# Kernel tuning notes

Hardware: AMD Instinct MI355X
Metric: run time of the kernel (lower is better)

Reference implementation:

```python
import jax, jax.numpy as jnp
import numpy as np

B, M, NV, H, D = 32, 64, 65, 960, 480
ROUNDS = 5
SCALE = D ** -0.5


def _self_att(x, m, qw, qb):
    # x: [B, P, Q, C] attention over Q within each (b, p); m: [B, P, Q]
    qkv = x @ qw.T + qb                      # [B,P,Q,3C]
    q, k, v = jnp.split(qkv, 3, axis=-1)
    # torch builds mask@mask^T/C from a C-times repeated mask == outer product of mask values
    am = m[..., :, None] * m[..., None, :]   # [B,P,Q,Q]
    a = jnp.einsum('bpqc,bpkc->bpqk', q, k) * SCALE
    a = jnp.where(am == 0, -10000.0, a)
    a = jax.nn.softmax(a, axis=-1)
    return jnp.einsum('bpqk,bpkc->bpqc', a, v)


def _attn_logits(x, mask, qw, qb):
    # Attention_logits.forward: attend over value axis, then over key axis
    x = _self_att(x, mask, qw, qb)
    x = _self_att(jnp.swapaxes(x, 1, 2), jnp.swapaxes(mask, 1, 2), qw, qb)
    return jnp.swapaxes(x, 1, 2)


def _biaffine(x1, x2, W, lw, lb):
    # torch.nn.Bilinear (no bias) on the MxN outer grid + Linear(cat(x1,x2)) with bias,
    # computed without materializing the repeated [B,M,N,2D] tensor.
    d = x1.shape[-1]
    bil = jnp.einsum('bmi,oij,bnj->bmno', x1, W, x2)
    lin = (x1 @ lw[:, :d].T)[:, :, None, :] + (x2 @ lw[:, d:].T)[:, None, :, :] + lb
    return bil + lin


def _rounds(key, value, km, vm, W, lw, lb, fw, fb, qw, qb):
    # shared structure of type_classifier / single_classifier (rounds=5, max pooling)
    lm = km[:, :, None] * vm[:, None, :]     # [B,M,N]
    logits = None
    for i in range(ROUNDS):
        logits = _biaffine(key, value, W, lw, lb)          # [B,M,N,out]
        if i < ROUNDS - 1:
            logits = logits @ fw.T + fb                    # [B,M,N,D]
            logits = _attn_logits(logits, lm, qw, qb)
            key = key + logits.max(axis=2)                 # max-pool over values
            value = value + logits.max(axis=1)             # max-pool over keys
        else:
            logits = logits * lm[..., None]
    return logits


def setup_inputs() -> dict:
    root = jax.random.key(0)
    ks = list(jax.random.split(root, 40))
    it = iter(ks)
    nrm = lambda sh, s=0.02: (jax.random.normal(next(it), sh, jnp.float32) * s)
    key = jax.random.normal(next(it), (B, M, H), jnp.float32)
    value = jax.random.normal(next(it), (B, NV, H), jnp.float32)
    klen = jax.random.randint(next(it), (B,), 1, M + 1)
    key_mask = (jnp.arange(M)[None, :] < klen[:, None]).astype(jnp.float32)
    vlen = jax.random.randint(next(it), (B,), 1, NV + 1)
    value_mask = (jnp.arange(NV)[None, :] < vlen[:, None]).astype(jnp.float32)
    return dict(
        key=key, value=value, key_mask=key_mask, value_mask=value_mask,
        w_kt=nrm((D, H)), b_kt=nrm((D,)), w_vt=nrm((D, H)), b_vt=nrm((D,)),
        w_km=nrm((D, H)), b_km=nrm((D,)), w_vm=nrm((D, H)), b_vm=nrm((D,)),
        w_ks=nrm((D, H)), b_ks=nrm((D,)), w_vs=nrm((D, H)), b_vs=nrm((D,)),
        bt_W=nrm((3, D, D)), bt_lw=nrm((3, 2 * D)), bt_lb=nrm((3,)),
        bi_W=nrm((2, D, D)), bi_lw=nrm((2, 2 * D)), bi_lb=nrm((2,)),
        w_ffnt=nrm((D, 3)), b_ffnt=nrm((D,)), w_ffn=nrm((D, 2)), b_ffn=nrm((D,)),
        qkvt_w=nrm((3 * D, D)), qkvt_b=nrm((3 * D,)),
        qkv_w=nrm((3 * D, D)), qkv_b=nrm((3 * D,)),
        w_cls=nrm((2, 2 * D)), b_cls=nrm((2,)),
    )


def reference(key, value, key_mask, value_mask,
              w_kt, b_kt, w_vt, b_vt, w_km, b_km, w_vm, b_vm,
              w_ks, b_ks, w_vs, b_vs,
              bt_W, bt_lw, bt_lb, bi_W, bi_lw, bi_lb,
              w_ffnt, b_ffnt, w_ffn, b_ffn,
              qkvt_w, qkvt_b, qkv_w, qkv_b, w_cls, b_cls):
    # --- type classifier ---
    kt = key @ w_kt.T + b_kt
    vt = value @ w_vt.T + b_vt
    type_logits = _rounds(kt, vt, key_mask, value_mask,
                          bt_W, bt_lw, bt_lb, w_ffnt, b_ffnt, qkvt_w, qkvt_b)  # [B,M,NV,3]
    # drop type token from values
    v1 = value[:, 1:, :]
    vm1 = value_mask[:, 1:]
    type_token = jax.nn.softmax(type_logits[:, :, 0], axis=-1)   # [B,M,3]
    key_type = jnp.argmax(type_token, axis=-1)
    type_single = key_type == 1
    # --- multi classifier (masks unused, as in original) ---
    km_f = key @ w_km.T + b_km
    vm_f = v1 @ w_vm.T + b_vm
    multi_logits = ((km_f @ w_cls[:, :D].T)[:, :, None, :]
                    + (vm_f @ w_cls[:, D:].T)[:, None, :, :] + b_cls)  # [B,M,M? -> B,64,64,2]
    # --- single classifier with key mask restricted to single-link keys ---
    km2 = (key_mask.astype(bool) & type_single).astype(key_mask.dtype)
    ks_f = key @ w_ks.T + b_ks
    vs_f = v1 @ w_vs.T + b_vs
    single_logits = _rounds(ks_f, vs_f, km2, vm1,
                            bi_W, bi_lw, bi_lb, w_ffn, b_ffn, qkv_w, qkv_b)  # [B,64,64,2]
    return (type_logits, multi_logits, single_logits)
```

## Files before the change

### kernel.cpp

```cpp
#include <hip/hip_runtime.h>
#include <math.h>

constexpr int NB = 32;
constexpr int NM = 64;
constexpr int NNV = 65;
constexpr int NH = 960;
constexpr int ND = 480;
constexpr float ATT_SCALE = 0.045643546458763842f;

constexpr int OF_Pq = 0;
constexpr int OF_cq = 4320;
constexpr int OF_Q2 = 5760;
constexpr int OF_V2 = OF_Q2 + 2*1440;
constexpr int OF_dq = 10080;
constexpr int OF_dv = OF_dq + 2*480;
constexpr int OF_S  = 11520;
constexpr int OF_u  = 11529;
constexpr int OF_r  = 11532;
constexpr int OF_w  = 11535;
constexpr int FOLD_SZ = 11552;

typedef float f32x4 __attribute__((ext_vector_type(4)));
typedef short s16x8 __attribute__((ext_vector_type(8)));

__device__ __forceinline__ float wave_sum(float v) {
#pragma unroll
  for (int d = 32; d; d >>= 1) v += __shfl_xor(v, d);
  return v;
}

__device__ __forceinline__ void split_bf16(float x, short& hi, short& lo) {
  union { float f; unsigned u; } a; a.f = x;
  unsigned uh = a.u + 0x7fffu + ((a.u >> 16) & 1u);
  hi = (short)(uh >> 16);
  union { unsigned u; float f; } b; b.u = ((unsigned)(unsigned short)hi) << 16;
  union { float f; unsigned u; } c; c.f = x - b.f;
  unsigned ul = c.u + 0x7fffu + ((c.u >> 16) & 1u);
  lo = (short)(ul >> 16);
}

struct ProjCfg {
  const float* X; const float* W; const float* bias; float* C;
  int R; int x0; int rpb; int xbs;
};
struct Proj6 { ProjCfg c[6]; };

constexpr int KP = 40;

__global__ __launch_bounds__(256) void k_projM(Proj6 P, int K)
{
  __shared__ unsigned short As_hi[64][KP], As_lo[64][KP];
  __shared__ unsigned short Bs_hi[48][KP], Bs_lo[48][KP];
  int p = blockIdx.x, total = gridDim.x;
  int q = total >> 3, r = total & 7;
  int xk = p & 7, idx = p >> 3;
  int lgc = (xk < r) ? (xk * (q + 1) + idx) : (r * (q + 1) + (xk - r) * q + idx);
  int mp = lgc / 10, nx = lgc - mp * 10;
  ProjCfg cfg; int my;
  if      (mp < 32)  { cfg = P.c[0]; my = mp; }
  else if (mp < 65)  { cfg = P.c[1]; my = mp - 32; }
  else if (mp < 97)  { cfg = P.c[2]; my = mp - 65; }
  else if (mp < 129) { cfg = P.c[3]; my = mp - 97; }
  else if (mp < 161) { cfg = P.c[4]; my = mp - 129; }
  else               { cfg = P.c[5]; my = mp - 161; }
  const int m0 = my * 64, n0 = nx * 48;
  const int tid = threadIdx.x;
  const int l6 = tid & 63, w = tid >> 6;
  const int lr = tid >> 2, kc = (tid & 3) * 8;
  const float* Arow = nullptr;
  {
    int rr = m0 + lr;
    if (rr < cfg.R) {
      int b = rr / cfg.rpb, r2 = rr - b * cfg.rpb;
      Arow = cfg.X + (size_t)b * cfg.xbs + (size_t)(cfg.x0 + r2) * K;
    }
  }
  const float* Brow = (lr < 48) ? (cfg.W + (size_t)(n0 + lr) * K) : nullptr;
  const int fr = l6 & 15, fk = (l6 >> 4) * 8;
  f32x4 acc0 = {0.f, 0.f, 0.f, 0.f}, acc1 = acc0, acc2 = acc0;
  for (int k0 = 0; k0 < K; k0 += 32) {
    float xs[8] = {0.f, 0.f, 0.f, 0.f, 0.f, 0.f, 0.f, 0.f};
    if (Arow) {
      float4 a0 = *(const float4*)(Arow + k0 + kc);
      float4 a1 = *(const float4*)(Arow + k0 + kc + 4);
      xs[0] = a0.x; xs[1] = a0.y; xs[2] = a0.z; xs[3] = a0.w;
      xs[4] = a1.x; xs[5] = a1.y; xs[6] = a1.z; xs[7] = a1.w;
    }
    s16x8 vh, vl;
#pragma unroll
    for (int e = 0; e < 8; ++e) { short h, lo2; split_bf16(xs[e], h, lo2); vh[e] = h; vl[e] = lo2; }
    *(s16x8*)&As_hi[lr][kc] = vh;
    *(s16x8*)&As_lo[lr][kc] = vl;
    if (Brow) {
      float4 b0 = *(const float4*)(Brow + k0 + kc);
      float4 b1 = *(const float4*)(Brow + k0 + kc + 4);
      float ys[8] = {b0.x, b0.y, b0.z, b0.w, b1.x, b1.y, b1.z, b1.w};
      s16x8 wh, wl;
#pragma unroll
      for (int e = 0; e < 8; ++e) { short h, lo2; split_bf16(ys[e], h, lo2); wh[e] = h; wl[e] = lo2; }
      *(s16x8*)&Bs_hi[lr][kc] = wh;
      *(s16x8*)&Bs_lo[lr][kc] = wl;
    }
    __syncthreads();
    s16x8 ah = *(const s16x8*)&As_hi[16 * w + fr][fk];
    s16x8 al = *(const s16x8*)&As_lo[16 * w + fr][fk];
    {
      s16x8 bh = *(const s16x8*)&Bs_hi[fr][fk];
      s16x8 bl = *(const s16x8*)&Bs_lo[fr][fk];
      acc0 = __builtin_amdgcn_mfma_f32_16x16x32_bf16(ah, bh, acc0, 0, 0, 0);
      acc0 = __builtin_amdgcn_mfma_f32_16x16x32_bf16(ah, bl, acc0, 0, 0, 0);
      acc0 = __builtin_amdgcn_mfma_f32_16x16x32_bf16(al, bh, acc0, 0, 0, 0);
    }
    {
      s16x8 bh = *(const s16x8*)&Bs_hi[16 + fr][fk];
      s16x8 bl = *(const s16x8*)&Bs_lo[16 + fr][fk];
      acc1 = __builtin_amdgcn_mfma_f32_16x16x32_bf16(ah, bh, acc1, 0, 0, 0);
      acc1 = __builtin_amdgcn_mfma_f32_16x16x32_bf16(ah, bl, acc1, 0, 0, 0);
      acc1 = __builtin_amdgcn_mfma_f32_16x16x32_bf16(al, bh, acc1, 0, 0, 0);
    }
    {
      s16x8 bh = *(const s16x8*)&Bs_hi[32 + fr][fk];
      s16x8 bl = *(const s16x8*)&Bs_lo[32 + fr][fk];
      acc2 = __builtin_amdgcn_mfma_f32_16x16x32_bf16(ah, bh, acc2, 0, 0, 0);
      acc2 = __builtin_amdgcn_mfma_f32_16x16x32_bf16(ah, bl, acc2, 0, 0, 0);
      acc2 = __builtin_amdgcn_mfma_f32_16x16x32_bf16(al, bh, acc2, 0, 0, 0);
    }
    __syncthreads();
  }
#pragma unroll
  for (int c = 0; c < 3; ++c) {
    f32x4 av = (c == 0) ? acc0 : (c == 1) ? acc1 : acc2;
    int n = n0 + 16 * c + fr;
    float bv = cfg.bias[n];
#pragma unroll
    for (int g = 0; g < 4; ++g) {
      int rr = m0 + 16 * w + (l6 >> 4) * 4 + g;
      if (rr < cfg.R) cfg.C[(size_t)rr * ND + n] = av[g] + bv;
    }
  }
}

__global__ __launch_bounds__(256) void k_tmpM(
    const float* __restrict__ Key, const float* __restrict__ W,
    float* __restrict__ T, int O)
{
  __shared__ unsigned short As_hi[64][KP], As_lo[64][KP];
  __shared__ unsigned short Bs_hi[48][KP], Bs_lo[48][KP];
  const int n0 = blockIdx.x * 48;
  const int o = blockIdx.y, b = blockIdx.z;
  const int tid = threadIdx.x;
  const int l6 = tid & 63, w = tid >> 6;
  const int lr = tid >> 2, kc = (tid & 3) * 8;
  const float* Arow = Key + (size_t)b * NM * ND + (size_t)lr * ND;
  const float* Wo = W + (size_t)o * ND * ND;
  const int fr = l6 & 15, fk = (l6 >> 4) * 8;
  f32x4 acc0 = {0.f, 0.f, 0.f, 0.f}, acc1 = acc0, acc2 = acc0;
  for (int k0 = 0; k0 < ND; k0 += 32) {
    {
      float4 a0 = *(const float4*)(Arow + k0 + kc);
      float4 a1 = *(const float4*)(Arow + k0 + kc + 4);
      float xs[8] = {a0.x, a0.y, a0.z, a0.w, a1.x, a1.y, a1.z, a1.w};
      s16x8 vh, vl;
#pragma unroll
      for (int e = 0; e < 8; ++e) { short h, lo2; split_bf16(xs[e], h, lo2); vh[e] = h; vl[e] = lo2; }
      *(s16x8*)&As_hi[lr][kc] = vh;
      *(s16x8*)&As_lo[lr][kc] = vl;
    }
    if (lr < 48) {
      s16x8 wh, wl;
#pragma unroll
      for (int e = 0; e < 8; ++e) {
        float x = Wo[(size_t)(k0 + kc + e) * ND + n0 + lr];
        short h, lo2; split_bf16(x, h, lo2); wh[e] = h; wl[e] = lo2;
      }
      *(s16x8*)&Bs_hi[lr][kc] = wh;
      *(s16x8*)&Bs_lo[lr][kc] = wl;
    }
    __syncthreads();
    s16x8 ah = *(const s16x8*)&As_hi[16 * w + fr][fk];
    s16x8 al = *(const s16x8*)&As_lo[16 * w + fr][fk];
    {
      s16x8 bh = *(const s16x8*)&Bs_hi[fr][fk];
      s16x8 bl = *(const s16x8*)&Bs_lo[fr][fk];
      acc0 = __builtin_amdgcn_mfma_f32_16x16x32_bf16(ah, bh, acc0, 0, 0, 0);
      acc0 = __builtin_amdgcn_mfma_f32_16x16x32_bf16(ah, bl, acc0, 0, 0, 0);
      acc0 = __builtin_amdgcn_mfma_f32_16x16x32_bf16(al, bh, acc0, 0, 0, 0);
    }
    {
      s16x8 bh = *(const s16x8*)&Bs_hi[16 + fr][fk];
      s16x8 bl = *(const s16x8*)&Bs_lo[16 + fr][fk];
      acc1 = __builtin_amdgcn_mfma_f32_16x16x32_bf16(ah, bh, acc1, 0, 0, 0);
      acc1 = __builtin_amdgcn_mfma_f32_16x16x32_bf16(ah, bl, acc1, 0, 0, 0);
      acc1 = __builtin_amdgcn_mfma_f32_16x16x32_bf16(al, bh, acc1, 0, 0, 0);
    }
    {
      s16x8 bh = *(const s16x8*)&Bs_hi[32 + fr][fk];
      s16x8 bl = *(const s16x8*)&Bs_lo[32 + fr][fk];
      acc2 = __builtin_amdgcn_mfma_f32_16x16x32_bf16(ah, bh, acc2, 0, 0, 0);
      acc2 = __builtin_amdgcn_mfma_f32_16x16x32_bf16(ah, bl, acc2, 0, 0, 0);
      acc2 = __builtin_amdgcn_mfma_f32_16x16x32_bf16(al, bh, acc2, 0, 0, 0);
    }
    __syncthreads();
  }
  float* C = T + ((size_t)(b * O + o) * NM) * ND;
#pragma unroll
  for (int c = 0; c < 3; ++c) {
    f32x4 av = (c == 0) ? acc0 : (c == 1) ? acc1 : acc2;
    int n = n0 + 16 * c + fr;
#pragma unroll
    for (int g = 0; g < 4; ++g) {
      int rr = 16 * w + (l6 >> 4) * 4 + g;
      C[(size_t)rr * ND + n] = av[g];
    }
  }
}

template <int O, int NVX>
__global__ __launch_bounds__(256) void k_bilatt0(
    const float* __restrict__ T, const float* __restrict__ Val,
    const float* __restrict__ linK, const float* __restrict__ linV,
    const float* __restrict__ lb, const float* __restrict__ F,
    const float* __restrict__ km, const float* __restrict__ vm,
    int vmOff, int vmStride, float* __restrict__ Y1)
{
  __shared__ float Ls[NVX][3];
  __shared__ float STs[NVX][3];
  __shared__ float hs[NVX], gs[NVX], mkj[NVX];
  __shared__ float Pm[NVX][66];
  __shared__ float rmx[NVX][3];
  __shared__ float rsum[NVX][3];
  __shared__ float ry[NVX][3][3];
  __shared__ float lvs[NVX][3];
  const int b = blockIdx.x >> 6, m = blockIdx.x & 63;
  const int tid = threadIdx.x;
  const int lane = tid & 63, w = tid >> 6;

  for (int j = tid; j < NVX; j += 256) {
    mkj[j] = vm[b * vmStride + vmOff + j];
#pragma unroll
    for (int o = 0; o < O; ++o) lvs[j][o] = linV[((size_t)b * NVX + j) * O + o];
  }
  float4 tsr[O][2];
#pragma unroll
  for (int o = 0; o < O; ++o) {
    const float4* trow = (const float4*)(T + (((size_t)b * O + o) * NM + m) * (size_t)ND);
    tsr[o][0] = trow[lane];
    tsr[o][1] = (lane < 56) ? trow[64 + lane] : make_float4(0.f, 0.f, 0.f, 0.f);
  }
  float lk[O];
#pragma unroll
  for (int o = 0; o < O; ++o) lk[o] = linK[((size_t)b * NM + m) * O + o] + lb[o];
  const float gm = km[b * NM + m];
  const bool gz = (gm == 0.f);

  for (int n = w; n < NVX; n += 4) {
    const float4* vrow = (const float4*)(Val + ((size_t)b * NVX + n) * (size_t)ND);
    float4 v0 = vrow[lane];
    float4 v1 = (lane < 56) ? vrow[64 + lane] : make_float4(0.f, 0.f, 0.f, 0.f);
    float a[3] = {0.f, 0.f, 0.f};
#pragma unroll
    for (int o = 0; o < O; ++o) {
      a[o] = v0.x * tsr[o][0].x + v0.y * tsr[o][0].y + v0.z * tsr[o][0].z + v0.w * tsr[o][0].w
           + v1.x * tsr[o][1].x + v1.y * tsr[o][1].y + v1.z * tsr[o][1].z + v1.w * tsr[o][1].w;
    }
#pragma unroll
    for (int o = 0; o < O; ++o) a[o] = wave_sum(a[o]);
    if (lane == 0) {
#pragma unroll
      for (int o = 0; o < O; ++o) Ls[n][o] = a[o] + lk[o] + lvs[n][o];
      if (O == 2) Ls[n][2] = 0.f;
    }
  }
  __syncthreads();
  const float* Sm = F + OF_S;
  const float u0 = F[OF_u], u1 = F[OF_u + 1], u2 = F[OF_u + 2];
  const float r0 = F[OF_r], r1 = F[OF_r + 1], r2 = F[OF_r + 2];
  const float wc = F[OF_w];
  if (tid < NVX) {
    int j = tid;
    float t0 = Ls[j][0], t1 = Ls[j][1], t2 = Ls[j][2];
    STs[j][0] = t0 * Sm[0] + t1 * Sm[3] + t2 * Sm[6];
    STs[j][1] = t0 * Sm[1] + t1 * Sm[4] + t2 * Sm[7];
    STs[j][2] = t0 * Sm[2] + t1 * Sm[5] + t2 * Sm[8];
    hs[j] = t0 * u0 + t1 * u1 + t2 * u2;
    gs[j] = t0 * r0 + t1 * r1 + t2 * r2;
  }
  __syncthreads();
  const bool act = tid < NVX * 3;
  int i = 0, qq = 0, jlo = 0, jhi = 0;
  float st0 = 0, st1 = 0, st2 = 0, hi = 0;
  bool rowz = true;
  if (act) {
    i = tid / 3; qq = tid - i * 3;
    jlo = qq * 22; jhi = (jlo + 22 < NVX) ? jlo + 22 : NVX;
    st0 = STs[i][0]; st1 = STs[i][1]; st2 = STs[i][2]; hi = hs[i];
    rowz = gz || (mkj[i] == 0.f);
    float mx = -3.0e38f;
    for (int j = jlo; j < jhi; ++j) {
      float s = st0 * Ls[j][0] + st1 * Ls[j][1] + hi + gs[j] + wc;
      if (O == 3) s += st2 * Ls[j][2];
      s = (rowz || mkj[j] == 0.f) ? -10000.f : ATT_SCALE * s;
      Pm[i][j] = s;
      mx = fmaxf(mx, s);
    }
    rmx[i][qq] = mx;
  }
  __syncthreads();
  if (act) {
    float mx = fmaxf(fmaxf(rmx[i][0], rmx[i][1]), rmx[i][2]);
    float sum = 0.f, y0 = 0.f, y1 = 0.f, y2 = 0.f;
    for (int j = jlo; j < jhi; ++j) {
      float pp = __expf(Pm[i][j] - mx);
      sum += pp; y0 += pp * Ls[j][0]; y1 += pp * Ls[j][1];
      if (O == 3) y2 += pp * Ls[j][2];
    }
    rsum[i][qq] = sum; ry[i][qq][0] = y0; ry[i][qq][1] = y1; ry[i][qq][2] = y2;
  }
  __syncthreads();
  if (tid < NVX) {
    int ii = tid;
    float sum = rsum[ii][0] + rsum[ii][1] + rsum[ii][2];
    float y0 = ry[ii][0][0] + ry[ii][1][0] + ry[ii][2][0];
    float y1 = ry[ii][0][1] + ry[ii][1][1] + ry[ii][2][1];
    float y2 = ry[ii][0][2] + ry[ii][1][2] + ry[ii][2][2];
    float inv = 1.f / sum;
    size_t ob = (((size_t)b * NM + m) * NVX + ii) * O;
    Y1[ob + 0] = y0 * inv;
    Y1[ob + 1] = y1 * inv;
    if (O == 3) Y1[ob + 2] = y2 * inv;
  }
}

template <int O, int NVX>
__global__ __launch_bounds__(256) void k_att1vupd(
    const float* __restrict__ Y1, float* __restrict__ Y2,
    const float* __restrict__ F,
    const float* __restrict__ km, const float* __restrict__ vm,
    int vmOff, int vmStride,
    float* __restrict__ valb, const float* __restrict__ lw,
    float* __restrict__ linV)
{
  __shared__ float Ys1[NM][3];
  __shared__ float STs[NM][3];
  __shared__ float hs[NM], gs[NM], mkm[NM];
  __shared__ float Pm[NM][66];
  __shared__ float rmx[NM][3];
  __shared__ float rsum[NM][3];
  __shared__ float ry[NM][3][3];
  __shared__ float Ys2[NM][3];
  __shared__ float vrow[ND];
  const int b = blockIdx.x / NVX, n = blockIdx.x - b * NVX;
  const int tid = threadIdx.x;
  for (int u = tid; u < NM * O; u += 256) {
    int mm = u % NM, o = u / NM;
    Ys1[mm][o] = Y1[(((size_t)b * NM + mm) * NVX + n) * O + o];
  }
  if (tid < NM) {
    mkm[tid] = km[b * NM + tid];
    if (O == 2) Ys1[tid][2] = 0.f;
  }
  const float gm = vm[b * vmStride + vmOff + n];
  const bool gz = (gm == 0.f);
  __syncthreads();
  const float* Sm = F + OF_S + 16;
  const float u0 = F[OF_u + 16], u1 = F[OF_u + 17], u2 = F[OF_u + 18];
  const float r0 = F[OF_r + 16], r1 = F[OF_r + 17], r2 = F[OF_r + 18];
  const float wc = F[OF_w + 16];
  if (tid < NM) {
    int j = tid;
    float t0 = Ys1[j][0], t1 = Ys1[j][1], t2 = Ys1[j][2];
    STs[j][0] = t0 * Sm[0] + t1 * Sm[3] + t2 * Sm[6];
    STs[j][1] = t0 * Sm[1] + t1 * Sm[4] + t2 * Sm[7];
    STs[j][2] = t0 * Sm[2] + t1 * Sm[5] + t2 * Sm[8];
    hs[j] = t0 * u0 + t1 * u1 + t2 * u2;
    gs[j] = t0 * r0 + t1 * r1 + t2 * r2;
  }
  __syncthreads();
  const bool act = tid < NM * 3;
  int i = 0, qq = 0, jlo = 0, jhi = 0;
  float st0 = 0, st1 = 0, st2 = 0, hi = 0;
  bool rowz = true;
  if (act) {
    i = tid / 3; qq = tid - i * 3;
    jlo = qq * 22; jhi = (jlo + 22 < NM) ? jlo + 22 : NM;
    st0 = STs[i][0]; st1 = STs[i][1]; st2 = STs[i][2]; hi = hs[i];
    rowz = gz || (mkm[i] == 0.f);
    float mx = -3.0e38f;
    for (int j = jlo; j < jhi; ++j) {
      float s = st0 * Ys1[j][0] + st1 * Ys1[j][1] + hi + gs[j] + wc;
      if (O == 3) s += st2 * Ys1[j][2];
      s = (rowz || mkm[j] == 0.f) ? -10000.f : ATT_SCALE * s;
      Pm[i][j] = s;
      mx = fmaxf(mx, s);
    }
    rmx[i][qq] = mx;
  }
  __syncthreads();
  if (act) {
    float mx = fmaxf(fmaxf(rmx[i][0], rmx[i][1]), rmx[i][2]);
    float sum = 0.f, y0 = 0.f, y1 = 0.f, y2 = 0.f;
    for (int j = jlo; j < jhi; ++j) {
      float pp = __expf(Pm[i][j] - mx);
      sum += pp; y0 += pp * Ys1[j][0]; y1 += pp * Ys1[j][1];
      if (O == 3) y2 += pp * Ys1[j][2];
    }
    rsum[i][qq] = sum; ry[i][qq][0] = y0; ry[i][qq][1] = y1; ry[i][qq][2] = y2;
  }
  __syncthreads();
  if (tid < NM) {
    int ii = tid;
    float sum = rsum[ii][0] + rsum[ii][1] + rsum[ii][2];
    float y0 = ry[ii][0][0] + ry[ii][1][0] + ry[ii][2][0];
    float y1 = ry[ii][0][1] + ry[ii][1][1] + ry[ii][2][1];
    float y2 = ry[ii][0][2] + ry[ii][1][2] + ry[ii][2][2];
    float inv = 1.f / sum;
    y0 *= inv; y1 *= inv; y2 *= inv;
    size_t ob = (((size_t)b * NVX + n) * NM + ii) * O;
    Y2[ob + 0] = y0; Y2[ob + 1] = y1;
    if (O == 3) Y2[ob + 2] = y2;
    Ys2[ii][0] = y0; Ys2[ii][1] = y1; Ys2[ii][2] = (O == 3) ? y2 : 0.f;
  }
  __syncthreads();
  const float* V2 = F + OF_V2;
  const float* dv = F + OF_dv;
  for (int d = tid; d < ND; d += 256) {
    float v0 = V2[d], v1 = V2[ND + d], v2 = (O == 3) ? V2[2 * ND + d] : 0.f;
    float mx = -3.0e38f;
    for (int j = 0; j < NM; ++j) {
      float s = Ys2[j][0] * v0 + Ys2[j][1] * v1;
      if (O == 3) s += Ys2[j][2] * v2;
      mx = fmaxf(mx, s);
    }
    size_t di = ((size_t)b * NVX + n) * ND + d;
    float nv = valb[di] + mx + dv[d];
    valb[di] = nv;
    vrow[d] = nv;
  }
  __syncthreads();
  const int wv = tid >> 6, lane = tid & 63;
  if (wv < O) {
    float acc = 0.f;
    for (int d = lane; d < ND; d += 64) acc += vrow[d] * lw[(size_t)wv * 2 * ND + ND + d];
    acc = wave_sum(acc);
    if (lane == 0) linV[((size_t)b * NVX + n) * O + wv] = acc;
  }
}

template <int O, int NVX>
__global__ __launch_bounds__(256) void k_kupd(
    const float* __restrict__ Y2, const float* __restrict__ F,
    float* __restrict__ keyb, const float* __restrict__ lw,
    float* __restrict__ linK)
{
  __shared__ float Ys[NVX][3];
  __shared__ float krow[ND];
  const int b = blockIdx.x >> 6, m = blockIdx.x & 63;
  const int tid = threadIdx.x;
  for (int u = tid; u < NVX * O; u += 256) {
    int j = u % NVX, o = u / NVX;
    Ys[j][o] = Y2[(((size_t)b * NVX + j) * NM + m) * O + o];
  }
  __syncthreads();
  const float* V2 = F + OF_V2;
  const float* dv = F + OF_dv;
  for (int d = tid; d < ND; d += 256) {
    float v0 = V2[d], v1 = V2[ND + d], v2 = (O == 3) ? V2[2 * ND + d] : 0.f;
    float mx = -3.0e38f;
    for (int j = 0; j < NVX; ++j) {
      float s = Ys[j][0] * v0 + Ys[j][1] * v1;
      if (O == 3) s += Ys[j][2] * v2;
      mx = fmaxf(mx, s);
    }
    size_t di = ((size_t)b * NM + m) * ND + d;
    float nv = keyb[di] + mx + dv[d];
    keyb[di] = nv;
    krow[d] = nv;
  }
  __syncthreads();
  const int wv = tid >> 6, lane = tid & 63;
  if (wv < O) {
    float acc = 0.f;
    for (int d = lane; d < ND; d += 64) acc += krow[d] * lw[(size_t)wv * 2 * ND + d];
    acc = wave_sum(acc);
    if (lane == 0) linK[((size_t)b * NM + m) * O + wv] = acc;
  }
}

template <int O, int NVX>
__global__ __launch_bounds__(256) void k_bilfin(
    const float* __restrict__ T, const float* __restrict__ Val,
    const float* __restrict__ linK, const float* __restrict__ linV,
    const float* __restrict__ lb, const float* __restrict__ km,
    const float* __restrict__ vm, int vmOff, int vmStride,
    float* __restrict__ Out)
{
  const int b = blockIdx.x >> 6, m = blockIdx.x & 63;
  const int tid = threadIdx.x;
  const int lane = tid & 63, w = tid >> 6;
  float4 tsr[O][2];
#pragma unroll
  for (int o = 0; o < O; ++o) {
    const float4* trow = (const float4*)(T + (((size_t)b * O + o) * NM + m) * (size_t)ND);
    tsr[o][0] = trow[lane];
    tsr[o][1] = (lane < 56) ? trow[64 + lane] : make_float4(0.f, 0.f, 0.f, 0.f);
  }
  float lk[O];
#pragma unroll
  for (int o = 0; o < O; ++o) lk[o] = linK[((size_t)b * NM + m) * O + o] + lb[o];
  const float kmv = km[b * NM + m];
  for (int n = w; n < NVX; n += 4) {
    const float4* vrow = (const float4*)(Val + ((size_t)b * NVX + n) * (size_t)ND);
    float4 v0 = vrow[lane];
    float4 v1 = (lane < 56) ? vrow[64 + lane] : make_float4(0.f, 0.f, 0.f, 0.f);
    float a[3] = {0.f, 0.f, 0.f};
#pragma unroll
    for (int o = 0; o < O; ++o) {
      a[o] = v0.x * tsr[o][0].x + v0.y * tsr[o][0].y + v0.z * tsr[o][0].z + v0.w * tsr[o][0].w
           + v1.x * tsr[o][1].x + v1.y * tsr[o][1].y + v1.z * tsr[o][1].z + v1.w * tsr[o][1].w;
    }
#pragma unroll
    for (int o = 0; o < O; ++o) a[o] = wave_sum(a[o]);
    if (lane == 0) {
      float msk = kmv * vm[b * vmStride + vmOff + n];
      size_t ob = (((size_t)b * NM + m) * NVX + n) * O;
#pragma unroll
      for (int o = 0; o < O; ++o)
        Out[ob + o] = (a[o] + lk[o] + linV[((size_t)b * NVX + n) * O + o]) * msk;
    }
  }
}

struct SpCfg { const float* X; const float* W; float* Out; int R; int O; int wStride; int wOff; };
__global__ __launch_bounds__(256) void k_sproj6(
    SpCfg s0, SpCfg s1, SpCfg s2, SpCfg s3, SpCfg s4, SpCfg s5)
{
  int z = blockIdx.y;
  SpCfg c = (z == 0) ? s0 : (z == 1) ? s1 : (z == 2) ? s2 : (z == 3) ? s3 : (z == 4) ? s4 : s5;
  int gid = blockIdx.x * 4 + (threadIdx.x >> 6);
  if (gid >= c.R * c.O) return;
  int lane = threadIdx.x & 63;
  int r = gid / c.O, o = gid - r * c.O;
  const float* x = c.X + (size_t)r * ND;
  const float* wp = c.W + (size_t)o * c.wStride + c.wOff;
  float acc = 0.f;
  for (int d = lane; d < ND; d += 64) acc += x[d] * wp[d];
  acc = wave_sum(acc);
  if (lane == 0) c.Out[gid] = acc;
}

struct FoldCfg { const float* fw; const float* fb; const float* qw; const float* qb; float* F; int O; };

__global__ __launch_bounds__(256) void k_fold1B(FoldCfg A, FoldCfg Bc)
{
  FoldCfg c = (blockIdx.y == 0) ? A : Bc;
  int O = c.O;
  int gid = blockIdx.x * 4 + (threadIdx.x >> 6);
  int lane = threadIdx.x & 63;
  if (gid >= 3 * ND) return;
  int part = gid / ND, cc0 = gid - part * ND;
  const float* qrow = c.qw + (size_t)(part * ND + cc0) * ND;
  float p0 = 0.f, p1 = 0.f, p2 = 0.f, cc = 0.f;
  for (int d = lane; d < ND; d += 64) {
    float q = qrow[d];
    p0 += c.fw[d * O + 0] * q;
    p1 += c.fw[d * O + 1] * q;
    if (O == 3) p2 += c.fw[d * O + 2] * q;
    cc += c.fb[d] * q;
  }
  p0 = wave_sum(p0); p1 = wave_sum(p1); p2 = wave_sum(p2); cc = wave_sum(cc);
  if (lane == 0) {
    c.F[OF_Pq + part * 1440 + 0 * ND + cc0] = p0;
    c.F[OF_Pq + part * 1440 + 1 * ND + cc0] = p1;
    c.F[OF_Pq + part * 1440 + 2 * ND + cc0] = (O == 3) ? p2 : 0.f;
    c.F[OF_cq + part * ND + cc0] = cc + c.qb[part * ND + cc0];
  }
}

__global__ __launch_bounds__(256) void k_fold2B(FoldCfg A, FoldCfg Bc)
{
  FoldCfg c = (blockIdx.y == 0) ? A : Bc;
  int O = c.O;
  float* F = c.F;
  int gid = blockIdx.x * 4 + (threadIdx.x >> 6);
  int lane = threadIdx.x & 63;
  if (gid < 3 * ND) {
    int part = gid / ND, cc0 = gid - part * ND;
    const float* qrow = c.qw + (size_t)(part * ND + cc0) * ND;
    const float* Pv = F + OF_Pq + 2 * 1440;
    const float* cv = F + OF_cq + 2 * ND;
    float p0 = 0.f, p1 = 0.f, p2 = 0.f, cc = 0.f;
    for (int d = lane; d < ND; d += 64) {
      float q = qrow[d];
      p0 += Pv[0 * ND + d] * q;
      p1 += Pv[1 * ND + d] * q;
      if (O == 3) p2 += Pv[2 * ND + d] * q;
      cc += cv[d] * q;
    }
    p0 = wave_sum(p0); p1 = wave_sum(p1); p2 = wave_sum(p2); cc = wave_sum(cc);
    if (lane == 0) {
      F[OF_Q2 + part * 1440 + 0 * ND + cc0] = p0;
      F[OF_Q2 + part * 1440 + 1 * ND + cc0] = p1;
      F[OF_Q2 + part * 1440 + 2 * ND + cc0] = (O == 3) ? p2 : 0.f;
      F[OF_dq + part * ND + cc0] = cc + c.qb[part * ND + cc0];
    }
  } else if (gid < 3 * ND + 16) {
    int s = gid - 3 * ND;
    const float* Pq = F + OF_Pq;
    const float* Pk = F + OF_Pq + 1440;
    const float* cq = F + OF_cq;
    const float* ck = F + OF_cq + ND;
    float acc = 0.f;
    if (s < 9) {
      int o = s / 3, op = s % 3;
      bool ok = (o < O) && (op < O);
      if (ok) for (int q = lane; q < ND; q += 64) acc += Pq[o * ND + q] * Pk[op * ND + q];
      acc = wave_sum(acc);
      if (lane == 0) F[OF_S + s] = ok ? acc : 0.f;
    } else if (s < 12) {
      int o = s - 9; bool ok = o < O;
      if (ok) for (int q = lane; q < ND; q += 64) acc += Pq[o * ND + q] * ck[q];
      acc = wave_sum(acc);
      if (lane == 0) F[OF_u + o] = ok ? acc : 0.f;
    } else if (s < 15) {
      int o = s - 12; bool ok = o < O;
      if (ok) for (int q = lane; q < ND; q += 64) acc += cq[q] * Pk[o * ND + q];
      acc = wave_sum(acc);
      if (lane == 0) F[OF_r + o] = ok ? acc : 0.f;
    } else {
      for (int q = lane; q < ND; q += 64) acc += cq[q] * ck[q];
      acc = wave_sum(acc);
      if (lane == 0) F[OF_w] = acc;
    }
  }
}

__global__ __launch_bounds__(256) void k_fold3B(FoldCfg A, FoldCfg Bc)
{
  FoldCfg c = (blockIdx.y == 0) ? A : Bc;
  int O = c.O;
  float* F = c.F;
  int s = blockIdx.x * 4 + (threadIdx.x >> 6);
  int lane = threadIdx.x & 63;
  if (s >= 16) return;
  const float* Q2 = F + OF_Q2;
  const float* K2 = F + OF_Q2 + 1440;
  const float* dq = F + OF_dq;
  const float* dk = F + OF_dq + ND;
  float acc = 0.f;
  if (s < 9) {
    int o = s / 3, op = s % 3;
    bool ok = (o < O) && (op < O);
    if (ok) for (int q = lane; q < ND; q += 64) acc += Q2[o * ND + q] * K2[op * ND + q];
    acc = wave_sum(acc);
    if (lane == 0) F[OF_S + 16 + s] = ok ? acc : 0.f;
  } else if (s < 12) {
    int o = s - 9; bool ok = o < O;
    if (ok) for (int q = lane; q < ND; q += 64) acc += Q2[o * ND + q] * dk[q];
    acc = wave_sum(acc);
    if (lane == 0) F[OF_u + 16 + o] = ok ? acc : 0.f;
  } else if (s < 15) {
    int o = s - 12; bool ok = o < O;
    if (ok) for (int q = lane; q < ND; q += 64) acc += dq[q] * K2[o * ND + q];
    acc = wave_sum(acc);
    if (lane == 0) F[OF_r + 16 + o] = ok ? acc : 0.f;
  } else {
    for (int q = lane; q < ND; q += 64) acc += dq[q] * dk[q];
    acc = wave_sum(acc);
    if (lane == 0) F[OF_w + 16] = acc;
  }
}

__global__ void k_type(const float* __restrict__ tl, const float* __restrict__ key_mask,
                       float* __restrict__ km2)
{
  int i = blockIdx.x * blockDim.x + threadIdx.x;
  if (i >= NB * NM) return;
  const float* p = tl + (size_t)i * NNV * 3;
  float l0 = p[0], l1 = p[1], l2 = p[2];
  int arg = 0;
  float best = l0;
  if (l1 > best) { best = l1; arg = 1; }
  if (l2 > best) { best = l2; arg = 2; }
  km2[i] = (key_mask[i] != 0.f && arg == 1) ? 1.f : 0.f;
}

__global__ void k_multi(const float* __restrict__ a, const float* __restrict__ bb,
                        const float* __restrict__ bc, float* __restrict__ out)
{
  int i = blockIdx.x * blockDim.x + threadIdx.x;
  if (i >= NB * NM * NM * 2) return;
  int c = i & 1;
  int t = i >> 1;
  int n = t % NM; t /= NM;
  int m = t % NM;
  int b = t / NM;
  out[i] = a[((size_t)b * NM + m) * 2 + c] + bb[((size_t)b * NM + n) * 2 + c] + bc[c];
}

template <int O, int NVX>
static void run_rounds(hipStream_t stream,
                       float* keyb, float* valb,
                       const float* kmp, const float* vmp, int vmOff, int vmStride,
                       const float* Wb, const float* lwp, const float* lbp,
                       float* fold, float* linK, float* linV,
                       float* tmp, float* Y1, float* Y2, float* outp)
{
  dim3 blk(256);
  for (int r = 0; r < 5; ++r) {
    k_tmpM<<<dim3(10, O, NB), blk, 0, stream>>>(keyb, Wb, tmp, O);
    if (r < 4) {
      k_bilatt0<O, NVX><<<dim3(NB * NM), blk, 0, stream>>>(
          tmp, valb, linK, linV, lbp, fold, kmp, vmp, vmOff, vmStride, Y1);
      k_att1vupd<O, NVX><<<dim3(NB * NVX), blk, 0, stream>>>(
          Y1, Y2, fold, kmp, vmp, vmOff, vmStride, valb, lwp, linV);
      k_kupd<O, NVX><<<dim3(NB * NM), blk, 0, stream>>>(Y2, fold, keyb, lwp, linK);
    } else {
      k_bilfin<O, NVX><<<dim3(NB * NM), blk, 0, stream>>>(
          tmp, valb, linK, linV, lbp, kmp, vmp, vmOff, vmStride, outp);
    }
  }
}

extern "C" void kernel_launch(void* const* d_in, const int* in_sizes, int n_in,
                              void* d_out, int out_size, void* d_ws, size_t ws_size,
                              hipStream_t stream)
{
  const float* key        = (const float*)d_in[0];
  const float* value      = (const float*)d_in[1];
  const float* key_mask   = (const float*)d_in[2];
  const float* value_mask = (const float*)d_in[3];
  const float* w_kt = (const float*)d_in[4];  const float* b_kt = (const float*)d_in[5];
  const float* w_vt = (const float*)d_in[6];  const float* b_vt = (const float*)d_in[7];
  const float* w_km = (const float*)d_in[8];  const float* b_km = (const float*)d_in[9];
  const float* w_vm = (const float*)d_in[10]; const float* b_vm = (const float*)d_in[11];
  const float* w_ks = (const float*)d_in[12]; const float* b_ks = (const float*)d_in[13];
  const float* w_vs = (const float*)d_in[14]; const float* b_vs = (const float*)d_in[15];
  const float* bt_W = (const float*)d_in[16]; const float* bt_lw = (const float*)d_in[17];
  const float* bt_lb = (const float*)d_in[18];
  const float* bi_W = (const float*)d_in[19]; const float* bi_lw = (const float*)d_in[20];
  const float* bi_lb = (const float*)d_in[21];
  const float* w_ffnt = (const float*)d_in[22]; const float* b_ffnt = (const float*)d_in[23];
  const float* w_ffn  = (const float*)d_in[24]; const float* b_ffn  = (const float*)d_in[25];
  const float* qkvt_w = (const float*)d_in[26]; const float* qkvt_b = (const float*)d_in[27];
  const float* qkv_w  = (const float*)d_in[28]; const float* qkv_b  = (const float*)d_in[29];
  const float* w_cls  = (const float*)d_in[30]; const float* b_cls  = (const float*)d_in[31];

  float* ws = (float*)d_ws;
  size_t off = 0;
  float* kt_t  = ws + off; off += (size_t)NB * NM * ND;
  float* vt_t  = ws + off; off += (size_t)NB * NNV * ND;
  float* kt_s  = ws + off; off += (size_t)NB * NM * ND;
  float* vt_s  = ws + off; off += (size_t)NB * NM * ND;
  float* tmp   = ws + off; off += (size_t)NB * 3 * NM * ND;
  float* Y1    = ws + off; off += (size_t)NB * NM * NNV * 3;
  float* Y2    = ws + off; off += (size_t)NB * NM * NNV * 3;
  float* linK_t = ws + off; off += (size_t)NB * NM * 3;
  float* linV_t = ws + off; off += (size_t)NB * NNV * 3;
  float* linK_s = ws + off; off += (size_t)NB * NM * 3;
  float* linV_s = ws + off; off += (size_t)NB * NM * 3;
  float* fold_t = ws + off; off += FOLD_SZ;
  float* fold_s = ws + off; off += FOLD_SZ;
  float* km2   = ws + off; off += (size_t)NB * NM;
  float* a2    = ws + off; off += (size_t)NB * NM * 2;
  float* b2    = ws + off; off += (size_t)NB * NM * 2;
  (void)off; (void)ws_size; (void)in_sizes; (void)n_in; (void)out_size;

  float* kmf = tmp;
  float* vmf = tmp + (size_t)NB * NM * ND;

  float* out_type   = (float*)d_out;
  float* out_multi  = out_type + (size_t)NB * NM * NNV * 3;
  float* out_single = out_multi + (size_t)NB * NM * NM * 2;

  dim3 blk(256);

  Proj6 P;
  P.c[0] = { key,   w_kt, b_kt, kt_t, NB * NM,  0, NM,  NM * NH };
  P.c[1] = { value, w_vt, b_vt, vt_t, NB * NNV, 0, NNV, NNV * NH };
  P.c[2] = { key,   w_ks, b_ks, kt_s, NB * NM,  0, NM,  NM * NH };
  P.c[3] = { value, w_vs, b_vs, vt_s, NB * NM,  1, NM,  NNV * NH };
  P.c[4] = { key,   w_km, b_km, kmf,  NB * NM,  0, NM,  NM * NH };
  P.c[5] = { value, w_vm, b_vm, vmf,  NB * NM,  1, NM,  NNV * NH };
  k_projM<<<dim3(193 * 10), blk, 0, stream>>>(P, NH);

  FoldCfg ft = { w_ffnt, b_ffnt, qkvt_w, qkvt_b, fold_t, 3 };
  FoldCfg fs = { w_ffn,  b_ffn,  qkv_w,  qkv_b,  fold_s, 2 };
  k_fold1B<<<dim3(360, 2), blk, 0, stream>>>(ft, fs);
  k_fold2B<<<dim3(364, 2), blk, 0, stream>>>(ft, fs);
  k_fold3B<<<dim3(4, 2), blk, 0, stream>>>(ft, fs);

  SpCfg s0 = { kt_t, bt_lw, linK_t, NB * NM,  3, 2 * ND, 0 };
  SpCfg s1 = { vt_t, bt_lw, linV_t, NB * NNV, 3, 2 * ND, ND };
  SpCfg s2 = { kt_s, bi_lw, linK_s, NB * NM,  2, 2 * ND, 0 };
  SpCfg s3 = { vt_s, bi_lw, linV_s, NB * NM,  2, 2 * ND, ND };
  SpCfg s4 = { kmf,  w_cls, a2,     NB * NM,  2, 2 * ND, 0 };
  SpCfg s5 = { vmf,  w_cls, b2,     NB * NM,  2, 2 * ND, ND };
  k_sproj6<<<dim3((NB * NNV * 3 + 3) / 4, 6), blk, 0, stream>>>(s0, s1, s2, s3, s4, s5);

  k_multi<<<dim3((NB * NM * NM * 2 + 255) / 256), blk, 0, stream>>>(a2, b2, b_cls, out_multi);

  run_rounds<3, NNV>(stream, kt_t, vt_t, key_mask, value_mask, 0, NNV,
                     bt_W, bt_lw, bt_lb, fold_t, linK_t, linV_t,
                     tmp, Y1, Y2, out_type);

  k_type<<<dim3(8), blk, 0, stream>>>(out_type, key_mask, km2);

  run_rounds<2, NM>(stream, kt_s, vt_s, km2, value_mask, 1, NNV,
                    bi_W, bi_lw, bi_lb, fold_s, linK_s, linV_s,
                    tmp, Y1, Y2, out_single);
}
```

Measured before the change: 1.097 ms.

## Merge value and key update kernels into one launch and fold type argmax into tmpM

```diff
diff --git a/kernel.cpp b/kernel.cpp
--- a/kernel.cpp
+++ b/kernel.cpp
@@ -142,13 +142,23 @@
 
 __global__ __launch_bounds__(256) void k_tmpM(
     const float* __restrict__ Key, const float* __restrict__ W,
-    float* __restrict__ T, int O)
+    float* __restrict__ T, int O,
+    const float* __restrict__ typeSrc, const float* __restrict__ keyMask,
+    float* __restrict__ km2, int doType)
 {
   __shared__ unsigned short As_hi[64][KP], As_lo[64][KP];
   __shared__ unsigned short Bs_hi[48][KP], Bs_lo[48][KP];
   const int n0 = blockIdx.x * 48;
   const int o = blockIdx.y, b = blockIdx.z;
   const int tid = threadIdx.x;
+  if (doType && blockIdx.x == 0 && blockIdx.y == 0 && tid < NM) {
+    const float* p = typeSrc + ((size_t)(b * NM + tid)) * NNV * 3;
+    float l0 = p[0], l1 = p[1], l2 = p[2];
+    int arg = 0; float best = l0;
+    if (l1 > best) { best = l1; arg = 1; }
+    if (l2 > best) { arg = 2; }
+    km2[b * NM + tid] = (keyMask[b * NM + tid] != 0.f && arg == 1) ? 1.f : 0.f;
+  }
   const int l6 = tid & 63, w = tid >> 6;
   const int lr = tid >> 2, kc = (tid & 3) * 8;
   const float* Arow = Key + (size_t)b * NM * ND + (size_t)lr * ND;
@@ -332,157 +342,166 @@
 }
 
 template <int O, int NVX>
-__global__ __launch_bounds__(256) void k_att1vupd(
-    const float* __restrict__ Y1, float* __restrict__ Y2,
-    const float* __restrict__ F,
+__global__ __launch_bounds__(256) void k_updB(
+    const float* __restrict__ Y1, const float* __restrict__ F,
     const float* __restrict__ km, const float* __restrict__ vm,
     int vmOff, int vmStride,
-    float* __restrict__ valb, const float* __restrict__ lw,
-    float* __restrict__ linV)
+    float* __restrict__ keyb, float* __restrict__ valb,
+    const float* __restrict__ lw,
+    float* __restrict__ linK, float* __restrict__ linV)
 {
   __shared__ float Ys1[NM][3];
   __shared__ float STs[NM][3];
   __shared__ float hs[NM], gs[NM], mkm[NM];
   __shared__ float Pm[NM][66];
-  __shared__ float rmx[NM][3];
-  __shared__ float rsum[NM][3];
-  __shared__ float ry[NM][3][3];
-  __shared__ float Ys2[NM][3];
-  __shared__ float vrow[ND];
-  const int b = blockIdx.x / NVX, n = blockIdx.x - b * NVX;
+  __shared__ float rmx[NM][3], rsum[NM][3], ry[NM][3][3];
+  __shared__ float Ys2[NVX][3];
+  __shared__ float drow[ND];
+  constexpr int RT = NVX + NM;
+  const int b = blockIdx.x / RT, rr = blockIdx.x - b * RT;
   const int tid = threadIdx.x;
-  for (int u = tid; u < NM * O; u += 256) {
-    int mm = u % NM, o = u / NM;
-    Ys1[mm][o] = Y1[(((size_t)b * NM + mm) * NVX + n) * O + o];
-  }
-  if (tid < NM) {
-    mkm[tid] = km[b * NM + tid];
-    if (O == 2) Ys1[tid][2] = 0.f;
-  }
-  const float gm = vm[b * vmStride + vmOff + n];
-  const bool gz = (gm == 0.f);
-  __syncthreads();
+  const float* V2 = F + OF_V2;
+  const float* dvp = F + OF_dv;
   const float* Sm = F + OF_S + 16;
   const float u0 = F[OF_u + 16], u1 = F[OF_u + 17], u2 = F[OF_u + 18];
   const float r0 = F[OF_r + 16], r1 = F[OF_r + 17], r2 = F[OF_r + 18];
   const float wc = F[OF_w + 16];
-  if (tid < NM) {
-    int j = tid;
-    float t0 = Ys1[j][0], t1 = Ys1[j][1], t2 = Ys1[j][2];
-    STs[j][0] = t0 * Sm[0] + t1 * Sm[3] + t2 * Sm[6];
-    STs[j][1] = t0 * Sm[1] + t1 * Sm[4] + t2 * Sm[7];
-    STs[j][2] = t0 * Sm[2] + t1 * Sm[5] + t2 * Sm[8];
-    hs[j] = t0 * u0 + t1 * u1 + t2 * u2;
-    gs[j] = t0 * r0 + t1 * r1 + t2 * r2;
-  }
-  __syncthreads();
-  const bool act = tid < NM * 3;
-  int i = 0, qq = 0, jlo = 0, jhi = 0;
-  float st0 = 0, st1 = 0, st2 = 0, hi = 0;
-  bool rowz = true;
-  if (act) {
-    i = tid / 3; qq = tid - i * 3;
-    jlo = qq * 22; jhi = (jlo + 22 < NM) ? jlo + 22 : NM;
-    st0 = STs[i][0]; st1 = STs[i][1]; st2 = STs[i][2]; hi = hs[i];
-    rowz = gz || (mkm[i] == 0.f);
-    float mx = -3.0e38f;
-    for (int j = jlo; j < jhi; ++j) {
-      float s = st0 * Ys1[j][0] + st1 * Ys1[j][1] + hi + gs[j] + wc;
-      if (O == 3) s += st2 * Ys1[j][2];
-      s = (rowz || mkm[j] == 0.f) ? -10000.f : ATT_SCALE * s;
-      Pm[i][j] = s;
-      mx = fmaxf(mx, s);
-    }
-    rmx[i][qq] = mx;
-  }
-  __syncthreads();
-  if (act) {
-    float mx = fmaxf(fmaxf(rmx[i][0], rmx[i][1]), rmx[i][2]);
-    float sum = 0.f, y0 = 0.f, y1 = 0.f, y2 = 0.f;
-    for (int j = jlo; j < jhi; ++j) {
-      float pp = __expf(Pm[i][j] - mx);
-      sum += pp; y0 += pp * Ys1[j][0]; y1 += pp * Ys1[j][1];
-      if (O == 3) y2 += pp * Ys1[j][2];
-    }
-    rsum[i][qq] = sum; ry[i][qq][0] = y0; ry[i][qq][1] = y1; ry[i][qq][2] = y2;
-  }
-  __syncthreads();
-  if (tid < NM) {
-    int ii = tid;
-    float sum = rsum[ii][0] + rsum[ii][1] + rsum[ii][2];
-    float y0 = ry[ii][0][0] + ry[ii][1][0] + ry[ii][2][0];
-    float y1 = ry[ii][0][1] + ry[ii][1][1] + ry[ii][2][1];
-    float y2 = ry[ii][0][2] + ry[ii][1][2] + ry[ii][2][2];
-    float inv = 1.f / sum;
-    y0 *= inv; y1 *= inv; y2 *= inv;
-    size_t ob = (((size_t)b * NVX + n) * NM + ii) * O;
-    Y2[ob + 0] = y0; Y2[ob + 1] = y1;
-    if (O == 3) Y2[ob + 2] = y2;
-    Ys2[ii][0] = y0; Ys2[ii][1] = y1; Ys2[ii][2] = (O == 3) ? y2 : 0.f;
-  }
-  __syncthreads();
-  const float* V2 = F + OF_V2;
-  const float* dv = F + OF_dv;
-  for (int d = tid; d < ND; d += 256) {
-    float v0 = V2[d], v1 = V2[ND + d], v2 = (O == 3) ? V2[2 * ND + d] : 0.f;
-    float mx = -3.0e38f;
-    for (int j = 0; j < NM; ++j) {
-      float s = Ys2[j][0] * v0 + Ys2[j][1] * v1;
-      if (O == 3) s += Ys2[j][2] * v2;
-      mx = fmaxf(mx, s);
-    }
-    size_t di = ((size_t)b * NVX + n) * ND + d;
-    float nv = valb[di] + mx + dv[d];
-    valb[di] = nv;
-    vrow[d] = nv;
-  }
-  __syncthreads();
-  const int wv = tid >> 6, lane = tid & 63;
-  if (wv < O) {
-    float acc = 0.f;
-    for (int d = lane; d < ND; d += 64) acc += vrow[d] * lw[(size_t)wv * 2 * ND + ND + d];
-    acc = wave_sum(acc);
-    if (lane == 0) linV[((size_t)b * NVX + n) * O + wv] = acc;
-  }
-}
-
-template <int O, int NVX>
-__global__ __launch_bounds__(256) void k_kupd(
-    const float* __restrict__ Y2, const float* __restrict__ F,
-    float* __restrict__ keyb, const float* __restrict__ lw,
-    float* __restrict__ linK)
-{
-  __shared__ float Ys[NVX][3];
-  __shared__ float krow[ND];
-  const int b = blockIdx.x >> 6, m = blockIdx.x & 63;
-  const int tid = threadIdx.x;
-  for (int u = tid; u < NVX * O; u += 256) {
-    int j = u % NVX, o = u / NVX;
-    Ys[j][o] = Y2[(((size_t)b * NVX + j) * NM + m) * O + o];
-  }
-  __syncthreads();
-  const float* V2 = F + OF_V2;
-  const float* dv = F + OF_dv;
-  for (int d = tid; d < ND; d += 256) {
-    float v0 = V2[d], v1 = V2[ND + d], v2 = (O == 3) ? V2[2 * ND + d] : 0.f;
-    float mx = -3.0e38f;
-    for (int j = 0; j < NVX; ++j) {
-      float s = Ys[j][0] * v0 + Ys[j][1] * v1;
-      if (O == 3) s += Ys[j][2] * v2;
-      mx = fmaxf(mx, s);
-    }
-    size_t di = ((size_t)b * NM + m) * ND + d;
-    float nv = keyb[di] + mx + dv[d];
-    keyb[di] = nv;
-    krow[d] = nv;
-  }
-  __syncthreads();
-  const int wv = tid >> 6, lane = tid & 63;
-  if (wv < O) {
-    float acc = 0.f;
-    for (int d = lane; d < ND; d += 64) acc += krow[d] * lw[(size_t)wv * 2 * ND + d];
-    acc = wave_sum(acc);
-    if (lane == 0) linK[((size_t)b * NM + m) * O + wv] = acc;
+  if (tid < NM) mkm[tid] = km[b * NM + tid];
+
+  if (rr < NVX) {
+    const int n = rr;
+    for (int u = tid; u < NM * O; u += 256) {
+      int mm = u % NM, o = u / NM;
+      Ys1[mm][o] = Y1[(((size_t)b * NM + mm) * NVX + n) * O + o];
+    }
+    if (tid < NM && O == 2) Ys1[tid][2] = 0.f;
+    const float gm = vm[b * vmStride + vmOff + n];
+    const bool gz = (gm == 0.f);
+    __syncthreads();
+    if (tid < NM) {
+      int j = tid;
+      float t0 = Ys1[j][0], t1 = Ys1[j][1], t2 = Ys1[j][2];
+      STs[j][0] = t0 * Sm[0] + t1 * Sm[3] + t2 * Sm[6];
+      STs[j][1] = t0 * Sm[1] + t1 * Sm[4] + t2 * Sm[7];
+      STs[j][2] = t0 * Sm[2] + t1 * Sm[5] + t2 * Sm[8];
+      hs[j] = t0 * u0 + t1 * u1 + t2 * u2;
+      gs[j] = t0 * r0 + t1 * r1 + t2 * r2;
+    }
+    __syncthreads();
+    const bool act = tid < NM * 3;
+    int i = 0, qq = 0, jlo = 0, jhi = 0;
+    float st0 = 0, st1 = 0, st2 = 0, hi = 0;
+    bool rowz = true;
+    if (act) {
+      i = tid / 3; qq = tid - i * 3;
+      jlo = qq * 22; jhi = (jlo + 22 < NM) ? jlo + 22 : NM;
+      st0 = STs[i][0]; st1 = STs[i][1]; st2 = STs[i][2]; hi = hs[i];
+      rowz = gz || (mkm[i] == 0.f);
+      float mx = -3.0e38f;
+      for (int j = jlo; j < jhi; ++j) {
+        float s = st0 * Ys1[j][0] + st1 * Ys1[j][1] + hi + gs[j] + wc;
+        if (O == 3) s += st2 * Ys1[j][2];
+        s = (rowz || mkm[j] == 0.f) ? -10000.f : ATT_SCALE * s;
+        Pm[i][j] = s;
+        mx = fmaxf(mx, s);
+      }
+      rmx[i][qq] = mx;
+    }
+    __syncthreads();
+    if (act) {
+      float mx = fmaxf(fmaxf(rmx[i][0], rmx[i][1]), rmx[i][2]);
+      float sum = 0.f, y0 = 0.f, y1 = 0.f, y2 = 0.f;
+      for (int j = jlo; j < jhi; ++j) {
+        float pp = __expf(Pm[i][j] - mx);
+        sum += pp; y0 += pp * Ys1[j][0]; y1 += pp * Ys1[j][1];
+        if (O == 3) y2 += pp * Ys1[j][2];
+      }
+      rsum[i][qq] = sum; ry[i][qq][0] = y0; ry[i][qq][1] = y1; ry[i][qq][2] = y2;
+    }
+    __syncthreads();
+    if (tid < NM) {
+      int ii = tid;
+      float sum = rsum[ii][0] + rsum[ii][1] + rsum[ii][2];
+      float y0 = ry[ii][0][0] + ry[ii][1][0] + ry[ii][2][0];
+      float y1 = ry[ii][0][1] + ry[ii][1][1] + ry[ii][2][1];
+      float y2 = ry[ii][0][2] + ry[ii][1][2] + ry[ii][2][2];
+      float inv = 1.f / sum;
+      Ys2[ii][0] = y0 * inv; Ys2[ii][1] = y1 * inv;
+      Ys2[ii][2] = (O == 3) ? y2 * inv : 0.f;
+    }
+    __syncthreads();
+    for (int d = tid; d < ND; d += 256) {
+      float v0 = V2[d], v1 = V2[ND + d], v2 = (O == 3) ? V2[2 * ND + d] : 0.f;
+      float mx = -3.0e38f;
+      for (int j = 0; j < NM; ++j) {
+        float s = Ys2[j][0] * v0 + Ys2[j][1] * v1;
+        if (O == 3) s += Ys2[j][2] * v2;
+        mx = fmaxf(mx, s);
+      }
+      size_t di = ((size_t)b * NVX + n) * ND + d;
+      float nv = valb[di] + mx + dvp[d];
+      valb[di] = nv;
+      drow[d] = nv;
+    }
+    __syncthreads();
+    const int wv = tid >> 6, lane = tid & 63;
+    if (wv < O) {
+      float acc = 0.f;
+      for (int d = lane; d < ND; d += 64) acc += drow[d] * lw[(size_t)wv * 2 * ND + ND + d];
+      acc = wave_sum(acc);
+      if (lane == 0) linV[((size_t)b * NVX + n) * O + wv] = acc;
+    }
+  } else {
+    const int m = rr - NVX;
+    __syncthreads();
+    const float qm = mkm[m];
+    for (int n = tid; n < NVX; n += 256) {
+      float gmv = vm[b * vmStride + vmOff + n];
+      bool rowz = (gmv == 0.f) || (qm == 0.f);
+      size_t mi = (((size_t)b * NM + m) * NVX + n) * O;
+      float Yi0 = Y1[mi], Yi1 = Y1[mi + 1], Yi2 = (O == 3) ? Y1[mi + 2] : 0.f;
+      float st0 = Yi0 * Sm[0] + Yi1 * Sm[3] + Yi2 * Sm[6];
+      float st1 = Yi0 * Sm[1] + Yi1 * Sm[4] + Yi2 * Sm[7];
+      float st2 = Yi0 * Sm[2] + Yi1 * Sm[5] + Yi2 * Sm[8];
+      float hi = Yi0 * u0 + Yi1 * u1 + Yi2 * u2;
+      float mx = -3.0e38f, sum = 0.f, y0 = 0.f, y1 = 0.f, y2 = 0.f;
+      for (int j = 0; j < NM; ++j) {
+        size_t ji = (((size_t)b * NM + j) * NVX + n) * O;
+        float t0 = Y1[ji], t1 = Y1[ji + 1], t2 = (O == 3) ? Y1[ji + 2] : 0.f;
+        float s = st0 * t0 + st1 * t1 + st2 * t2 + hi
+                + (t0 * r0 + t1 * r1 + t2 * r2) + wc;
+        s = (rowz || mkm[j] == 0.f) ? -10000.f : ATT_SCALE * s;
+        float nm2 = fmaxf(mx, s);
+        float pp = __expf(s - nm2), cg = __expf(mx - nm2);
+        sum = sum * cg + pp; y0 = y0 * cg + pp * t0; y1 = y1 * cg + pp * t1; y2 = y2 * cg + pp * t2;
+        mx = nm2;
+      }
+      float inv = 1.f / sum;
+      Ys2[n][0] = y0 * inv; Ys2[n][1] = y1 * inv;
+      Ys2[n][2] = (O == 3) ? y2 * inv : 0.f;
+    }
+    __syncthreads();
+    for (int d = tid; d < ND; d += 256) {
+      float v0 = V2[d], v1 = V2[ND + d], v2 = (O == 3) ? V2[2 * ND + d] : 0.f;
+      float mx = -3.0e38f;
+      for (int j = 0; j < NVX; ++j) {
+        float s = Ys2[j][0] * v0 + Ys2[j][1] * v1;
+        if (O == 3) s += Ys2[j][2] * v2;
+        mx = fmaxf(mx, s);
+      }
+      size_t di = ((size_t)b * NM + m) * ND + d;
+      float nv = keyb[di] + mx + dvp[d];
+      keyb[di] = nv;
+      drow[d] = nv;
+    }
+    __syncthreads();
+    const int wv = tid >> 6, lane = tid & 63;
+    if (wv < O) {
+      float acc = 0.f;
+      for (int d = lane; d < ND; d += 64) acc += drow[d] * lw[(size_t)wv * 2 * ND + d];
+      acc = wave_sum(acc);
+      if (lane == 0) linK[((size_t)b * NM + m) * O + wv] = acc;
+    }
   }
 }
 
@@ -670,20 +689,6 @@
   }
 }
 
-__global__ void k_type(const float* __restrict__ tl, const float* __restrict__ key_mask,
-                       float* __restrict__ km2)
-{
-  int i = blockIdx.x * blockDim.x + threadIdx.x;
-  if (i >= NB * NM) return;
-  const float* p = tl + (size_t)i * NNV * 3;
-  float l0 = p[0], l1 = p[1], l2 = p[2];
-  int arg = 0;
-  float best = l0;
-  if (l1 > best) { best = l1; arg = 1; }
-  if (l2 > best) { best = l2; arg = 2; }
-  km2[i] = (key_mask[i] != 0.f && arg == 1) ? 1.f : 0.f;
-}
-
 __global__ void k_multi(const float* __restrict__ a, const float* __restrict__ bb,
                         const float* __restrict__ bc, float* __restrict__ out)
 {
@@ -703,17 +708,18 @@
                        const float* kmp, const float* vmp, int vmOff, int vmStride,
                        const float* Wb, const float* lwp, const float* lbp,
                        float* fold, float* linK, float* linV,
-                       float* tmp, float* Y1, float* Y2, float* outp)
+                       float* tmp, float* Y1, float* outp,
+                       const float* typeSrc, const float* keyMaskG, float* km2G, int doType)
 {
   dim3 blk(256);
   for (int r = 0; r < 5; ++r) {
-    k_tmpM<<<dim3(10, O, NB), blk, 0, stream>>>(keyb, Wb, tmp, O);
+    k_tmpM<<<dim3(10, O, NB), blk, 0, stream>>>(keyb, Wb, tmp, O,
+        typeSrc, keyMaskG, km2G, (r == 0) ? doType : 0);
     if (r < 4) {
       k_bilatt0<O, NVX><<<dim3(NB * NM), blk, 0, stream>>>(
           tmp, valb, linK, linV, lbp, fold, kmp, vmp, vmOff, vmStride, Y1);
-      k_att1vupd<O, NVX><<<dim3(NB * NVX), blk, 0, stream>>>(
-          Y1, Y2, fold, kmp, vmp, vmOff, vmStride, valb, lwp, linV);
-      k_kupd<O, NVX><<<dim3(NB * NM), blk, 0, stream>>>(Y2, fold, keyb, lwp, linK);
+      k_updB<O, NVX><<<dim3(NB * (NVX + NM)), blk, 0, stream>>>(
+          Y1, fold, kmp, vmp, vmOff, vmStride, keyb, valb, lwp, linK, linV);
     } else {
       k_bilfin<O, NVX><<<dim3(NB * NM), blk, 0, stream>>>(
           tmp, valb, linK, linV, lbp, kmp, vmp, vmOff, vmStride, outp);
@@ -747,23 +753,24 @@
 
   float* ws = (float*)d_ws;
   size_t off = 0;
-  float* kt_t  = ws + off; off += (size_t)NB * NM * ND;
-  float* vt_t  = ws + off; off += (size_t)NB * NNV * ND;
-  float* kt_s  = ws + off; off += (size_t)NB * NM * ND;
-  float* vt_s  = ws + off; off += (size_t)NB * NM * ND;
-  float* tmp   = ws + off; off += (size_t)NB * 3 * NM * ND;
-  float* Y1    = ws + off; off += (size_t)NB * NM * NNV * 3;
-  float* Y2    = ws + off; off += (size_t)NB * NM * NNV * 3;
-  float* linK_t = ws + off; off += (size_t)NB * NM * 3;
-  float* linV_t = ws + off; off += (size_t)NB * NNV * 3;
-  float* linK_s = ws + off; off += (size_t)NB * NM * 3;
-  float* linV_s = ws + off; off += (size_t)NB * NM * 3;
-  float* fold_t = ws + off; off += FOLD_SZ;
-  float* fold_s = ws + off; off += FOLD_SZ;
-  float* km2   = ws + off; off += (size_t)NB * NM;
-  float* a2    = ws + off; off += (size_t)NB * NM * 2;
-  float* b2    = ws + off; off += (size_t)NB * NM * 2;
-  (void)off; (void)ws_size; (void)in_sizes; (void)n_in; (void)out_size;
+  auto alloc = [&](size_t nfloat) { float* p = ws + off; off += (nfloat + 3) & ~(size_t)3; return p; };
+
+  float* kt_t   = alloc((size_t)NB * NM * ND);
+  float* vt_t   = alloc((size_t)NB * NNV * ND);
+  float* kt_s   = alloc((size_t)NB * NM * ND);
+  float* vt_s   = alloc((size_t)NB * NM * ND);
+  float* tmp    = alloc((size_t)NB * 3 * NM * ND);
+  float* Y1     = alloc((size_t)NB * NM * NNV * 3);
+  float* linK_t = alloc((size_t)NB * NM * 3);
+  float* linV_t = alloc((size_t)NB * NNV * 3);
+  float* linK_s = alloc((size_t)NB * NM * 3);
+  float* linV_s = alloc((size_t)NB * NM * 3);
+  float* fold_t = alloc(FOLD_SZ);
+  float* fold_s = alloc(FOLD_SZ);
+  float* km2    = alloc((size_t)NB * NM);
+  float* a2     = alloc((size_t)NB * NM * 2);
+  float* b2     = alloc((size_t)NB * NM * 2);
+  (void)ws_size; (void)in_sizes; (void)n_in; (void)out_size;
 
   float* kmf = tmp;
   float* vmf = tmp + (size_t)NB * NM * ND;
@@ -801,11 +808,9 @@
 
   run_rounds<3, NNV>(stream, kt_t, vt_t, key_mask, value_mask, 0, NNV,
                      bt_W, bt_lw, bt_lb, fold_t, linK_t, linV_t,
-                     tmp, Y1, Y2, out_type);
-
-  k_type<<<dim3(8), blk, 0, stream>>>(out_type, key_mask, km2);
+                     tmp, Y1, out_type, nullptr, nullptr, nullptr, 0);
 
   run_rounds<2, NM>(stream, kt_s, vt_s, km2, value_mask, 1, NNV,
                     bi_W, bi_lw, bi_lb, fold_s, linK_s, linV_s,
-                    tmp, Y1, Y2, out_single);
-}
+                    tmp, Y1, out_single, out_type, key_mask, km2, 1);
+}
```

After: 1.272 ms. +15.9%, slower.
